# Kernel tuning notes

Hardware: AMD Instinct MI355X
Metric: run time of the kernel (lower is better)

The kernel has to match this reference:

```python
import jax, jax.numpy as jnp
import numpy as np

SIGMA = 1.0  # RBF kernel bandwidth (init kwarg)

def setup_inputs() -> dict:
    key = jax.random.key(0)
    ks = jax.random.split(key, 5)
    B, N, D_in, D_emb = 8, 2048, 1024, 512
    scale = 1.0 / np.sqrt(D_in)
    return {
        "x": jax.random.normal(ks[0], (B, N, D_in), jnp.float32),
        "W_mu": jax.random.normal(ks[1], (D_emb, D_in), jnp.float32) * scale,
        "b_mu": jax.random.normal(ks[2], (D_emb,), jnp.float32) * scale,
        "W_logvar": jax.random.normal(ks[3], (D_emb, D_in), jnp.float32) * scale,
        "b_logvar": jax.random.normal(ks[4], (D_emb,), jnp.float32) * scale,
    }

def reference(x, W_mu, b_mu, W_logvar, b_logvar):
    # dual linear heads: (B,N,D_in) -> (B,N,D_emb)
    mu = jnp.einsum('bnd,ed->bne', x, W_mu) + b_mu
    logvar = jnp.einsum('bnd,ed->bne', x, W_logvar) + b_logvar
    sigma = jnp.exp(0.5 * logvar)
    # RBF kernel matrix K(x, x): (B,N,N) via ||xi||^2 + ||xj||^2 - 2 xi.xj
    sq = jnp.sum(x * x, axis=-1)                       # (B,N)
    gram = jnp.einsum('bnd,bmd->bnm', x, x)            # (B,N,N)
    dist = sq[:, :, None] + sq[:, None, :] - 2.0 * gram
    K = jnp.exp(-dist / (2.0 * SIGMA ** 2))            # (B,N,N)
    cov_diag = jnp.diagonal(K, axis1=1, axis2=2)       # (B,N) == exp(0) = 1
    sigma_adjusted = sigma * cov_diag[..., None]       # (B,N,D_emb)
    return (mu, sigma_adjusted)
```

## Files before the change

kernel.cpp:

```cpp
#include <hip/hip_runtime.h>
#include <hip/hip_bf16.h>
#include <math.h>

typedef __bf16 bf16;
typedef __attribute__((ext_vector_type(4))) float f32x4;
typedef __attribute__((ext_vector_type(8))) bf16 bf16x8;

#define M_TOT 16384
#define K_TOT 1024
#define D_EMB 512
#define NT 32

__global__ __launch_bounds__(256) void cvt_w_img(
    const float* __restrict__ W_mu, const float* __restrict__ W_logvar,
    bf16* __restrict__ img)
{
    const int c  = blockIdx.x * 256 + threadIdx.x;
    const int l  = c & 63;
    const int kt = (c >> 6) & 31;
    const int es = c >> 11;
    const int col = es * 16 + (l & 15);
    const int k0  = kt * 32 + (l >> 4) * 8;
    const float* s = (col < D_EMB) ? (W_mu + (size_t)col * K_TOT + k0)
                                   : (W_logvar + (size_t)(col - D_EMB) * K_TOT + k0);
    f32x4 a = ((const f32x4*)s)[0];
    f32x4 b = ((const f32x4*)s)[1];
    bf16x8 o;
    o[0] = (bf16)a[0]; o[1] = (bf16)a[1]; o[2] = (bf16)a[2]; o[3] = (bf16)a[3];
    o[4] = (bf16)b[0]; o[5] = (bf16)b[1]; o[6] = (bf16)b[2]; o[7] = (bf16)b[3];
    *(bf16x8*)(img + (size_t)c * 8) = o;
}

__global__ __launch_bounds__(512, 2) void gpe_gemm(
    const float* __restrict__ x,
    const bf16* __restrict__ wimg,
    const float* __restrict__ b_mu,
    const float* __restrict__ b_logvar,
    float* __restrict__ out)
{
    __shared__ __align__(16) bf16 Alds[2 * 256 * 32];

    const int tid  = threadIdx.x;
    const int lane = tid & 63;
    const int wid  = tid >> 6;
    const int wr   = wid >> 2;
    const int wc   = wid & 3;

    const int bid = blockIdx.x;
    const int swz = (bid & 7) * 32 + (bid >> 3);
    const int bn  = swz & 3;
    const int bm  = swz >> 2;

    const int r_l  = tid >> 1;
    const int half = tid & 1;
    const float* __restrict__ Asrc = x + (size_t)(bm * 256 + r_l) * K_TOT + half * 16;
    const int wxor  = (r_l >> 1) & 3;
    const int woff0 = r_l * 32 + ((half * 2 + 0) ^ wxor) * 8;
    const int woff1 = r_l * 32 + ((half * 2 + 1) ^ wxor) * 8;

    const int fr  = lane & 15;
    const int g16 = lane >> 4;
    const int rsl = (g16 ^ ((fr >> 1) & 3)) * 8;
    const int rA  = wr * 128 + fr;

    const bf16* __restrict__ bb =
        wimg + (size_t)(bn * 16 + wc * 4) * 16384 + lane * 8;

    f32x4 acc[8][4];
#pragma unroll
    for (int m = 0; m < 8; ++m)
#pragma unroll
        for (int n = 0; n < 4; ++n)
            acc[m][n] = (f32x4){0.f, 0.f, 0.f, 0.f};

    f32x4 regA[4];
    auto gloadA = [&](int t) {
#pragma unroll
        for (int j = 0; j < 4; ++j)
            regA[j] = *(const f32x4*)(Asrc + t * 32 + j * 4);
    };
    auto cwA = [&](bf16* abase) {
        bf16x8 w0, w1;
#pragma unroll
        for (int j = 0; j < 4; ++j) {
            w0[j]     = (bf16)regA[0][j];
            w0[j + 4] = (bf16)regA[1][j];
            w1[j]     = (bf16)regA[2][j];
            w1[j + 4] = (bf16)regA[3][j];
        }
        *(bf16x8*)&abase[woff0] = w0;
        *(bf16x8*)&abase[woff1] = w1;
    };
    auto gloadB = [&](int t, bf16x8 (&bv)[4]) {
#pragma unroll
        for (int n = 0; n < 4; ++n)
            bv[n] = *(const bf16x8*)(bb + (size_t)n * 16384 + t * 512);
    };

    bf16x8 bvA[4], bvB[4];

    gloadA(0);
    asm volatile("s_waitcnt vmcnt(0)" ::: "memory");
    cwA(Alds);
    gloadB(0, bvA);
    gloadA(1);
    asm volatile("s_waitcnt lgkmcnt(0)" ::: "memory");
    __builtin_amdgcn_s_barrier();

#define TILE_BODY(T, P, BVC, BVN)                                              \
    {                                                                          \
        const int t = (T);                                                     \
        bf16* Ab  = Alds + (P) * 8192;                                         \
        bf16* Abn = Alds + ((P) ^ 1) * 8192;                                   \
        if (t + 1 < NT) asm volatile("s_waitcnt vmcnt(4)" ::: "memory");       \
        else            asm volatile("s_waitcnt vmcnt(0)" ::: "memory");       \
        if (t + 1 < NT) {                                                      \
            gloadB(t + 1, BVN);                                                \
            asm volatile("s_waitcnt vmcnt(4)" ::: "memory");                   \
            cwA(Abn);                                                          \
            if (t + 2 < NT) gloadA(t + 2);                                     \
        }                                                                      \
        bf16x8 af[8];                                                          \
        _Pragma("unroll")                                                      \
        for (int m = 0; m < 8; ++m)                                            \
            af[m] = *(const bf16x8*)&Ab[(rA + m * 16) * 32 + rsl];             \
        asm volatile("s_waitcnt lgkmcnt(0)" ::: "memory");                     \
        __builtin_amdgcn_s_barrier();                                          \
        __builtin_amdgcn_s_setprio(1);                                         \
        _Pragma("unroll")                                                      \
        for (int n = 0; n < 4; ++n)                                            \
            _Pragma("unroll")                                                  \
            for (int m = 0; m < 8; ++m)                                        \
                acc[m][n] = __builtin_amdgcn_mfma_f32_16x16x32_bf16(           \
                    af[m], BVC[n], acc[m][n], 0, 0, 0);                        \
        __builtin_amdgcn_s_setprio(0);                                         \
    }

    for (int tt = 0; tt < NT; tt += 2) {
        TILE_BODY(tt,     0, bvA, bvB)
        TILE_BODY(tt + 1, 1, bvB, bvA)
    }
#undef TILE_BODY

    const bool is_mu = (bn < 2);
    const float* __restrict__ bias = is_mu ? b_mu : b_logvar;
    const int cb = (bn & 1) * 256;
    float* __restrict__ obase = is_mu ? out : (out + (size_t)M_TOT * D_EMB);

#pragma unroll
    for (int m = 0; m < 8; ++m) {
        const int row0 = bm * 256 + wr * 128 + m * 16 + g16 * 4;
#pragma unroll
        for (int n = 0; n < 4; ++n) {
            const int c = cb + wc * 64 + n * 16 + fr;
            const float bvs = bias[c];
#pragma unroll
            for (int j = 0; j < 4; ++j) {
                float v = acc[m][n][j] + bvs;
                if (!is_mu) v = __expf(0.5f * v);
                obase[(size_t)(row0 + j) * D_EMB + c] = v;
            }
        }
    }
}

#define LDS_STRIDE 40
__global__ __launch_bounds__(256) void gpe_gemm_fb(
    const float* __restrict__ x, const float* __restrict__ W_mu,
    const float* __restrict__ b_mu, const float* __restrict__ W_logvar,
    const float* __restrict__ b_logvar, float* __restrict__ out)
{
    __shared__ __align__(16) bf16 As[128][LDS_STRIDE];
    __shared__ __align__(16) bf16 Bs[128][LDS_STRIDE];
    typedef __attribute__((ext_vector_type(4))) bf16 bf16x4;
    const int tid = threadIdx.x, lane = tid & 63, wid = tid >> 6;
    const int wr = wid >> 1, wc = wid & 1;
    const int bn = blockIdx.x & 7, bm = blockIdx.x >> 3;
    const int ebase = bn * 128;
    const bool is_mu = (ebase < D_EMB);
    const float* Wp = is_mu ? (W_mu + (size_t)ebase * K_TOT)
                            : (W_logvar + (size_t)(ebase - D_EMB) * K_TOT);
    const float* bias = is_mu ? b_mu : b_logvar;
    const int cbase = is_mu ? ebase : (ebase - D_EMB);
    float* obase = is_mu ? out : (out + (size_t)M_TOT * D_EMB);
    const float* Ap = x + (size_t)(bm * 128) * K_TOT;
    f32x4 acc[4][4];
#pragma unroll
    for (int m = 0; m < 4; ++m)
#pragma unroll
        for (int n = 0; n < 4; ++n) acc[m][n] = (f32x4){0.f, 0.f, 0.f, 0.f};
    const int fr = lane & 15, fk = (lane >> 4) * 8;
    const int arow = wr * 64 + fr, brow = wc * 64 + fr;
    for (int kt = 0; kt < K_TOT / 32; ++kt) {
        const int k0 = kt * 32;
#pragma unroll
        for (int s = 0; s < 4; ++s) {
            const int idx = s * 256 + tid;
            const int row = idx >> 3, col = (idx & 7) << 2;
            f32x4 va = *reinterpret_cast<const f32x4*>(Ap + (size_t)row * K_TOT + k0 + col);
            f32x4 vb = *reinterpret_cast<const f32x4*>(Wp + (size_t)row * K_TOT + k0 + col);
            bf16x4 ha, hb;
#pragma unroll
            for (int j = 0; j < 4; ++j) { ha[j] = (bf16)va[j]; hb[j] = (bf16)vb[j]; }
            *reinterpret_cast<bf16x4*>(&As[row][col]) = ha;
            *reinterpret_cast<bf16x4*>(&Bs[row][col]) = hb;
        }
        __syncthreads();
        bf16x8 af[4], bfv[4];
#pragma unroll
        for (int m = 0; m < 4; ++m)
            af[m] = *reinterpret_cast<const bf16x8*>(&As[arow + m * 16][fk]);
#pragma unroll
        for (int n = 0; n < 4; ++n)
            bfv[n] = *reinterpret_cast<const bf16x8*>(&Bs[brow + n * 16][fk]);
#pragma unroll
        for (int m = 0; m < 4; ++m)
#pragma unroll
            for (int n = 0; n < 4; ++n)
                acc[m][n] = __builtin_amdgcn_mfma_f32_16x16x32_bf16(af[m], bfv[n], acc[m][n], 0, 0, 0);
        __syncthreads();
    }
#pragma unroll
    for (int m = 0; m < 4; ++m) {
        const int rbase = bm * 128 + wr * 64 + m * 16 + (lane >> 4) * 4;
#pragma unroll
        for (int n = 0; n < 4; ++n) {
            const int c = cbase + wc * 64 + n * 16 + (lane & 15);
            const float bv = bias[c];
#pragma unroll
            for (int j = 0; j < 4; ++j) {
                float v = acc[m][n][j] + bv;
                if (!is_mu) v = __expf(0.5f * v);
                obase[(size_t)(rbase + j) * D_EMB + c] = v;
            }
        }
    }
}

extern "C" void kernel_launch(void* const* d_in, const int* in_sizes, int n_in,
                              void* d_out, int out_size, void* d_ws, size_t ws_size,
                              hipStream_t stream) {
    const float* x        = (const float*)d_in[0];
    const float* W_mu     = (const float*)d_in[1];
    const float* b_mu     = (const float*)d_in[2];
    const float* W_logvar = (const float*)d_in[3];
    const float* b_logvar = (const float*)d_in[4];
    float* out = (float*)d_out;

    const size_t ws_needed = (size_t)1024 * 1024 * sizeof(bf16);

    if (ws_size >= ws_needed) {
        bf16* wimg = (bf16*)d_ws;
        cvt_w_img<<<512, 256, 0, stream>>>(W_mu, W_logvar, wimg);
        gpe_gemm<<<256, 512, 0, stream>>>(x, wimg, b_mu, b_logvar, out);
    } else {
        gpe_gemm_fb<<<1024, 256, 0, stream>>>(x, W_mu, b_mu, W_logvar, b_logvar, out);
    }
}
```

Baseline: 51.12 us.

## Halve GEMM M-tile to 128 rows and double grid for occupancy

The main bf16 MFMA GEMM now uses a 128-row A tile per block instead of 256, halving the accumulator registers and LDS, and launches 512 blocks with a launch bound allowing 4 blocks per CU. The B-fragment double buffering across tiles is replaced by a single register set loaded after the MFMAs, and the wait becomes a full vmcnt(0). The aim is better occupancy and more blocks to fill the CUs (256 blocks against 256 CUs was a single wave). The cost is that each W fragment is reused over fewer rows, so total B traffic doubles, and the simpler pipeline exposes more load latency.

```diff
diff --git a/kernel.cpp b/kernel.cpp
--- a/kernel.cpp
+++ b/kernel.cpp
@@ -31,14 +31,14 @@
     *(bf16x8*)(img + (size_t)c * 8) = o;
 }
 
-__global__ __launch_bounds__(512, 2) void gpe_gemm(
+__global__ __launch_bounds__(512, 4) void gpe_gemm(
     const float* __restrict__ x,
     const bf16* __restrict__ wimg,
     const float* __restrict__ b_mu,
     const float* __restrict__ b_logvar,
     float* __restrict__ out)
 {
-    __shared__ __align__(16) bf16 Alds[2 * 256 * 32];
+    __shared__ __align__(16) bf16 Alds[2 * 128 * 32];
 
     const int tid  = threadIdx.x;
     const int lane = tid & 63;
@@ -47,100 +47,85 @@
     const int wc   = wid & 3;
 
     const int bid = blockIdx.x;
-    const int swz = (bid & 7) * 32 + (bid >> 3);
+    const int swz = (bid & 7) * 64 + (bid >> 3);
     const int bn  = swz & 3;
     const int bm  = swz >> 2;
 
-    const int r_l  = tid >> 1;
-    const int half = tid & 1;
-    const float* __restrict__ Asrc = x + (size_t)(bm * 256 + r_l) * K_TOT + half * 16;
-    const int wxor  = (r_l >> 1) & 3;
-    const int woff0 = r_l * 32 + ((half * 2 + 0) ^ wxor) * 8;
-    const int woff1 = r_l * 32 + ((half * 2 + 1) ^ wxor) * 8;
+    const int r_l = tid >> 2;
+    const int q   = tid & 3;
+    const float* __restrict__ Asrc = x + (size_t)(bm * 128 + r_l) * K_TOT + q * 8;
+    const int woff = r_l * 32 + ((q ^ ((r_l >> 1) & 3)) << 3);
 
     const int fr  = lane & 15;
     const int g16 = lane >> 4;
-    const int rsl = (g16 ^ ((fr >> 1) & 3)) * 8;
-    const int rA  = wr * 128 + fr;
 
     const bf16* __restrict__ bb =
         wimg + (size_t)(bn * 16 + wc * 4) * 16384 + lane * 8;
 
-    f32x4 acc[8][4];
-#pragma unroll
-    for (int m = 0; m < 8; ++m)
+    f32x4 acc[4][4];
+#pragma unroll
+    for (int m = 0; m < 4; ++m)
 #pragma unroll
         for (int n = 0; n < 4; ++n)
             acc[m][n] = (f32x4){0.f, 0.f, 0.f, 0.f};
 
-    f32x4 regA[4];
+    f32x4 regA[2];
+    bf16x8 bv[4];
+
     auto gloadA = [&](int t) {
-#pragma unroll
-        for (int j = 0; j < 4; ++j)
-            regA[j] = *(const f32x4*)(Asrc + t * 32 + j * 4);
+        regA[0] = *(const f32x4*)(Asrc + t * 32);
+        regA[1] = *(const f32x4*)(Asrc + t * 32 + 4);
     };
     auto cwA = [&](bf16* abase) {
-        bf16x8 w0, w1;
-#pragma unroll
-        for (int j = 0; j < 4; ++j) {
-            w0[j]     = (bf16)regA[0][j];
-            w0[j + 4] = (bf16)regA[1][j];
-            w1[j]     = (bf16)regA[2][j];
-            w1[j + 4] = (bf16)regA[3][j];
-        }
-        *(bf16x8*)&abase[woff0] = w0;
-        *(bf16x8*)&abase[woff1] = w1;
+        bf16x8 w;
+#pragma unroll
+        for (int j = 0; j < 4; ++j) { w[j] = (bf16)regA[0][j]; w[j + 4] = (bf16)regA[1][j]; }
+        *(bf16x8*)&abase[woff] = w;
     };
-    auto gloadB = [&](int t, bf16x8 (&bv)[4]) {
+    auto gloadB = [&](int t) {
 #pragma unroll
         for (int n = 0; n < 4; ++n)
             bv[n] = *(const bf16x8*)(bb + (size_t)n * 16384 + t * 512);
     };
-
-    bf16x8 bvA[4], bvB[4];
 
     gloadA(0);
     asm volatile("s_waitcnt vmcnt(0)" ::: "memory");
     cwA(Alds);
-    gloadB(0, bvA);
     gloadA(1);
+    gloadB(0);
     asm volatile("s_waitcnt lgkmcnt(0)" ::: "memory");
     __builtin_amdgcn_s_barrier();
 
-#define TILE_BODY(T, P, BVC, BVN)                                              \
-    {                                                                          \
-        const int t = (T);                                                     \
-        bf16* Ab  = Alds + (P) * 8192;                                         \
-        bf16* Abn = Alds + ((P) ^ 1) * 8192;                                   \
-        if (t + 1 < NT) asm volatile("s_waitcnt vmcnt(4)" ::: "memory");       \
-        else            asm volatile("s_waitcnt vmcnt(0)" ::: "memory");       \
-        if (t + 1 < NT) {                                                      \
-            gloadB(t + 1, BVN);                                                \
-            asm volatile("s_waitcnt vmcnt(4)" ::: "memory");                   \
-            cwA(Abn);                                                          \
-            if (t + 2 < NT) gloadA(t + 2);                                     \
-        }                                                                      \
-        bf16x8 af[8];                                                          \
-        _Pragma("unroll")                                                      \
-        for (int m = 0; m < 8; ++m)                                            \
-            af[m] = *(const bf16x8*)&Ab[(rA + m * 16) * 32 + rsl];             \
-        asm volatile("s_waitcnt lgkmcnt(0)" ::: "memory");                     \
-        __builtin_amdgcn_s_barrier();                                          \
-        __builtin_amdgcn_s_setprio(1);                                         \
-        _Pragma("unroll")                                                      \
-        for (int n = 0; n < 4; ++n)                                            \
-            _Pragma("unroll")                                                  \
-            for (int m = 0; m < 8; ++m)                                        \
-                acc[m][n] = __builtin_amdgcn_mfma_f32_16x16x32_bf16(           \
-                    af[m], BVC[n], acc[m][n], 0, 0, 0);                        \
-        __builtin_amdgcn_s_setprio(0);                                         \
-    }
-
-    for (int tt = 0; tt < NT; tt += 2) {
-        TILE_BODY(tt,     0, bvA, bvB)
-        TILE_BODY(tt + 1, 1, bvB, bvA)
-    }
-#undef TILE_BODY
+    for (int t = 0; t < NT; ++t) {
+        const int p = t & 1;
+        bf16* Ab  = Alds + p * 4096;
+        bf16* Abn = Alds + (p ^ 1) * 4096;
+
+        asm volatile("s_waitcnt vmcnt(0)" ::: "memory");
+        if (t + 1 < NT) {
+            cwA(Abn);
+            if (t + 2 < NT) gloadA(t + 2);
+        }
+
+        bf16x8 af[4];
+#pragma unroll
+        for (int m = 0; m < 4; ++m) {
+            const int row = wr * 64 + m * 16 + fr;
+            af[m] = *(const bf16x8*)&Ab[row * 32 + ((g16 ^ ((row >> 1) & 3)) << 3)];
+        }
+        asm volatile("s_waitcnt lgkmcnt(0)" ::: "memory");
+        __builtin_amdgcn_s_barrier();
+
+        __builtin_amdgcn_s_setprio(1);
+#pragma unroll
+        for (int n = 0; n < 4; ++n)
+#pragma unroll
+            for (int m = 0; m < 4; ++m)
+                acc[m][n] = __builtin_amdgcn_mfma_f32_16x16x32_bf16(af[m], bv[n], acc[m][n], 0, 0, 0);
+        __builtin_amdgcn_s_setprio(0);
+
+        if (t + 1 < NT) gloadB(t + 1);
+    }
 
     const bool is_mu = (bn < 2);
     const float* __restrict__ bias = is_mu ? b_mu : b_logvar;
@@ -148,8 +133,8 @@
     float* __restrict__ obase = is_mu ? out : (out + (size_t)M_TOT * D_EMB);
 
 #pragma unroll
-    for (int m = 0; m < 8; ++m) {
-        const int row0 = bm * 256 + wr * 128 + m * 16 + g16 * 4;
+    for (int m = 0; m < 4; ++m) {
+        const int row0 = bm * 128 + wr * 64 + m * 16 + g16 * 4;
 #pragma unroll
         for (int n = 0; n < 4; ++n) {
             const int c = cb + wc * 64 + n * 16 + fr;
@@ -252,7 +237,7 @@
     if (ws_size >= ws_needed) {
         bf16* wimg = (bf16*)d_ws;
         cvt_w_img<<<512, 256, 0, stream>>>(W_mu, W_logvar, wimg);
-        gpe_gemm<<<256, 512, 0, stream>>>(x, wimg, b_mu, b_logvar, out);
+        gpe_gemm<<<512, 512, 0, stream>>>(x, wimg, b_mu, b_logvar, out);
     } else {
         gpe_gemm_fb<<<1024, 256, 0, stream>>>(x, W_mu, b_mu, W_logvar, b_logvar, out);
     }
```

Result: no change. 51.84 us (+1.4%).
